# Kernel optimization log

Hardware: AMD Instinct MI355X
Metric: run time of the kernel (lower is better)

The kernel has to match this reference:

```python
import jax, jax.numpy as jnp
import numpy as np

N_NODES = 50000
N_EDGES = 400000
H = 128
L = 3
T = 2
FEAT = 4
N_DATA = 40000


def setup_inputs() -> dict:
    key = jax.random.key(0)
    ks = jax.random.split(key, 12)
    s = lambda k, shape, fan: jax.random.normal(k, shape, dtype=jnp.float32) / np.sqrt(fan)
    inp = {
        'x': jax.random.normal(ks[0], (N_NODES, FEAT), dtype=jnp.float32),
        'edge_index': jax.random.randint(ks[1], (2, N_EDGES), 0, N_NODES, dtype=jnp.int64) if jax.config.jax_enable_x64 else jax.random.randint(ks[1], (2, N_EDGES), 0, N_NODES).astype(jnp.int32),
        'edge_type': jax.random.randint(ks[2], (N_EDGES,), 0, T).astype(jnp.int32),
        'n_data': N_DATA,
        'W_in': s(ks[3], (FEAT, H), FEAT),
        'b_in': jnp.zeros((H,), jnp.float32),
        'W1': s(ks[4], (L, T, 2 * H, H), 2 * H),
        'b1': jnp.zeros((L, T, H), jnp.float32),
        'W2': s(ks[5], (L, T, H, H), H),
        'b2': jnp.zeros((L, T, H), jnp.float32),
        'W_ih': s(ks[6], (L, H, 3 * H), H),
        'b_ih': jnp.zeros((L, 3 * H), jnp.float32),
        'W_hh': s(ks[7], (L, H, 3 * H), H),
        'b_hh': jnp.zeros((L, 3 * H), jnp.float32),
        'Wr1': s(ks[8], (H, H), H),
        'br1': jnp.zeros((H,), jnp.float32),
        'Wr2': s(ks[9], (H, 1), H),
        'br2': jnp.zeros((1,), jnp.float32),
    }
    return inp


def _gru_cell(agg, h, W_ih, b_ih, W_hh, b_hh):
    # torch GRUCell: gates ordered (r, z, n)
    gi = agg @ W_ih + b_ih  # [N, 3H]
    gh = h @ W_hh + b_hh    # [N, 3H]
    i_r, i_z, i_n = jnp.split(gi, 3, axis=-1)
    h_r, h_z, h_n = jnp.split(gh, 3, axis=-1)
    r = jax.nn.sigmoid(i_r + h_r)
    z = jax.nn.sigmoid(i_z + h_z)
    n = jnp.tanh(i_n + r * h_n)
    return (1.0 - z) * n + z * h


def reference(x, edge_index, edge_type, n_data, W_in, b_in, W1, b1, W2, b2,
              W_ih, b_ih, W_hh, b_hh, Wr1, br1, Wr2, br2):
    num_nodes = x.shape[0]
    h = jax.nn.relu(x @ W_in + b_in)  # input_proj (dropout = identity in eval)
    src, dst = edge_index[0], edge_index[1]
    n_layers, n_types = W1.shape[0], W1.shape[1]
    for l in range(n_layers):
        cat = jnp.concatenate([h[src], h[dst]], axis=1)  # [E, 2H]
        msgs = jnp.zeros((cat.shape[0], h.shape[1]), dtype=h.dtype)
        for t in range(n_types):
            m_t = jax.nn.relu(cat @ W1[l, t] + b1[l, t]) @ W2[l, t] + b2[l, t]
            msgs = jnp.where((edge_type == t)[:, None], m_t, msgs)
        agg = jax.ops.segment_sum(msgs, dst, num_segments=num_nodes)  # scatter_add
        h = _gru_cell(agg, h, W_ih[l], b_ih[l], W_hh[l], b_hh[l])
    data_emb = h[:n_data]  # node_type==0 nodes are the first n_data nodes
    out = jax.nn.relu(data_emb @ Wr1 + br1) @ Wr2 + br2  # readout
    return out[:, 0]
```

## Files before the change

### kernel.cpp

```cpp
#include <hip/hip_runtime.h>
#include <math.h>


#define H 128
#define TE2 128
#define MS2 132
#define HS  136
#define FEAT 4
#define WG_PER_LAYER 196608
#define WR_TOTAL 32768

typedef __bf16 bf16x8 __attribute__((ext_vector_type(8)));
typedef __bf16 bf16x4 __attribute__((ext_vector_type(4)));
typedef float  f32x4  __attribute__((ext_vector_type(4)));

__global__ __launch_bounds__(256) void k_input(
    const float* __restrict__ x, const float* __restrict__ Win,
    const float* __restrict__ bin, float* __restrict__ h,
    __bf16* __restrict__ hb, int n_nodes)
{
    int idx = blockIdx.x * 256 + threadIdx.x;
    if (idx >= n_nodes * H) return;
    int n = idx >> 7, j = idx & 127;
    float acc = bin[j];
#pragma unroll
    for (int f = 0; f < FEAT; f++)
        acc += x[n * FEAT + f] * Win[f * H + j];
    float v = fmaxf(acc, 0.f);
    h[idx] = v;
    hb[idx] = (__bf16)v;
}

__global__ __launch_bounds__(256) void k_wconv(
    const float* __restrict__ W1, const float* __restrict__ W2,
    __bf16* __restrict__ Wsw)
{
    int gid = blockIdx.x * 256 + threadIdx.x;
    const int per_lt = 12 * 4096;
    if (gid >= 6 * per_lt) return;
    int lt = gid / per_lt, rem = gid % per_lt;
    int chunk = rem >> 12;
    int within = rem & 4095;
    int ct = within >> 9;
    int lane = (within >> 3) & 63;
    int j = within & 7;
    int r = lane & 15, quad = lane >> 4;
    int n = ct * 16 + r;
    float v;
    if (chunk < 8) {
        int k = chunk * 32 + quad * 8 + j;
        v = W1[((size_t)lt * 256 + k) * 128 + n];
    } else {
        int k = (chunk - 8) * 32 + quad * 8 + j;
        v = W2[((size_t)lt * 128 + k) * 128 + n];
    }
    Wsw[gid] = (__bf16)v;
}

__global__ __launch_bounds__(256) void k_wgconv(
    const float* __restrict__ Wih, const float* __restrict__ Whh,
    __bf16* __restrict__ Wg)
{
    int gid = blockIdx.x * 256 + threadIdx.x;
    if (gid >= 3 * WG_PER_LAYER) return;
    int layer = gid / WG_PER_LAYER, rem = gid % WG_PER_LAYER;
    int t = rem & 7;
    int lane = (rem >> 3) & 63;
    int jtg = (rem >> 9) % 24;
    int mk = rem / 12288;
    int kc = mk & 3;
    int msplit = mk >> 2;
    int mat = msplit >> 1, split = msplit & 1;
    int r = lane & 15, quad = lane >> 4;
    int k = kc * 32 + quad * 8 + t;
    int n = jtg * 16 + r;
    const float* W = (mat ? Whh : Wih) + (size_t)layer * 128 * 384;
    float v = W[(size_t)k * 384 + n];
    __bf16 hi = (__bf16)v;
    Wg[gid] = split ? (__bf16)(v - (float)hi) : hi;
}

__global__ __launch_bounds__(256) void k_wrconv(
    const float* __restrict__ Wr1, __bf16* __restrict__ Wr1s)
{
    int gid = blockIdx.x * 256 + threadIdx.x;
    if (gid >= WR_TOTAL) return;
    int t = gid & 7;
    int lane = (gid >> 3) & 63;
    int jtg = (gid >> 9) & 7;
    int kc = (gid >> 12) & 3;
    int split = gid >> 14;
    int r = lane & 15, quad = lane >> 4;
    int k = kc * 32 + quad * 8 + t;
    int n = jtg * 16 + r;
    float v = Wr1[(size_t)k * H + n];
    __bf16 hi = (__bf16)v;
    Wr1s[gid] = split ? (__bf16)(v - (float)hi) : hi;
}

__global__ __launch_bounds__(256) void k_hist(
    const int* __restrict__ et, const int* __restrict__ dst,
    int* __restrict__ cnt, int n_edges, int nn)
{
    int i = blockIdx.x * 256 + threadIdx.x;
    if (i < n_edges) atomicAdd(&cnt[et[i] * nn + dst[i]], 1);
}

__global__ __launch_bounds__(1024) void k_scan1(
    const int* __restrict__ cnt, int* __restrict__ bsum, int n)
{
    int i = blockIdx.x * 1024 + threadIdx.x;
    int v = (i < n) ? cnt[i] : 0;
#pragma unroll
    for (int off = 32; off > 0; off >>= 1) v += __shfl_down(v, off, 64);
    __shared__ int ws[16];
    int lane = threadIdx.x & 63, w = threadIdx.x >> 6;
    if (lane == 0) ws[w] = v;
    __syncthreads();
    if (threadIdx.x < 16) {
        int x = ws[threadIdx.x];
#pragma unroll
        for (int off = 8; off > 0; off >>= 1) x += __shfl_down(x, off, 64);
        if (threadIdx.x == 0) bsum[blockIdx.x] = x;
    }
}

__global__ __launch_bounds__(128) void k_scan2(
    int* __restrict__ bsum, int* __restrict__ offs, int nb, int n)
{
    int lane = threadIdx.x & 63, w = threadIdx.x >> 6;
    int v = (threadIdx.x < nb) ? bsum[threadIdx.x] : 0;
    int orig = v;
#pragma unroll
    for (int off = 1; off < 64; off <<= 1) {
        int t = __shfl_up(v, off, 64);
        if (lane >= off) v += t;
    }
    __shared__ int w0sum;
    if (threadIdx.x == 63) w0sum = v;
    __syncthreads();
    int ex = v - orig + (w ? w0sum : 0);
    if (threadIdx.x < nb) bsum[threadIdx.x] = ex;
    if (threadIdx.x == nb - 1) offs[n] = ex + orig;
}

__global__ __launch_bounds__(1024) void k_scan3(
    const int* __restrict__ cnt, const int* __restrict__ bsum,
    int* __restrict__ offs, int n)
{
    int i = blockIdx.x * 1024 + threadIdx.x;
    int v = (i < n) ? cnt[i] : 0;
    int orig = v;
    int lane = threadIdx.x & 63, w = threadIdx.x >> 6;
#pragma unroll
    for (int off = 1; off < 64; off <<= 1) {
        int t = __shfl_up(v, off, 64);
        if (lane >= off) v += t;
    }
    __shared__ int ws[16];
    if (lane == 63) ws[w] = v;
    __syncthreads();
    if (threadIdx.x < 16) {
        int x = ws[threadIdx.x];
#pragma unroll
        for (int off = 1; off < 16; off <<= 1) {
            int t = __shfl_up(x, off, 64);
            if (lane >= off) x += t;
        }
        ws[threadIdx.x] = x;
    }
    __syncthreads();
    int wbase = w ? ws[w - 1] : 0;
    if (i < n) offs[i] = bsum[blockIdx.x] + wbase + v - orig;
}

__global__ __launch_bounds__(256) void k_place(
    const int* __restrict__ et, const int* __restrict__ dst,
    const int* __restrict__ offs, int* __restrict__ cnt,
    int* __restrict__ bucket, int n_edges, int nn)
{
    int i = blockIdx.x * 256 + threadIdx.x;
    if (i < n_edges) {
        int key = et[i] * nn + dst[i];
        int p = atomicAdd(&cnt[key], -1) - 1;
        bucket[offs[key] + p] = i;
    }
}

__global__ __launch_bounds__(512, 4) void k_msg(
    const __bf16* __restrict__ hb,
    const int* __restrict__ bucket, const int* __restrict__ offs,
    const int* __restrict__ src, const int* __restrict__ dst,
    const __bf16* __restrict__ Wsw, const float* __restrict__ b1l,
    const float* __restrict__ b2l,
    float* __restrict__ agg, int n_edges, int nn)
{
    const int t = blockIdx.y;
    const int c0 = offs[nn];
    const int cnt = t ? (n_edges - c0) : c0;
    const int base = t ? c0 : 0;
    const int start = blockIdx.x * TE2;
    if (start >= cnt) return;

    const __bf16* __restrict__ W = Wsw + (size_t)t * 12 * 4096;
    const float*  __restrict__ b1 = b1l + t * H;
    const float*  __restrict__ b2 = b2l + t * H;

    __shared__ __bf16 sW[4096];
    __shared__ float  sMsg[TE2 * MS2];
    __shared__ int    sDstV[TE2];

    const int tid  = threadIdx.x;
    const int lane = tid & 63;
    const int w    = tid >> 6;
    const int r    = lane & 15;
    const int quad = lane >> 4;

    f32x4 wreg[12];
#pragma unroll
    for (int c = 0; c < 12; c++)
        wreg[c] = *(const f32x4*)(W + c * 4096 + tid * 8);

    if (tid < TE2) {
        int i = start + tid;
        sDstV[tid] = (i < cnt) ? dst[bucket[base + i]] : -1;
    }

    int ei = start + w * 16 + r;
    int e = bucket[base + (ei < cnt ? ei : cnt - 1)];
    const __bf16* aps = hb + (size_t)src[e] * H;
    const __bf16* apd = hb + (size_t)dst[e] * H;

    bf16x8 afS[4];
#pragma unroll
    for (int i = 0; i < 4; i++)
        afS[i] = *(const bf16x8*)(aps + i * 32 + quad * 8);

    __syncthreads();

    f32x4 acc[8];
#pragma unroll
    for (int ct = 0; ct < 8; ct++) acc[ct] = (f32x4){0.f, 0.f, 0.f, 0.f};

    bf16x8 afD[4];
#pragma unroll
    for (int kc = 0; kc < 8; kc++) {
        __syncthreads();
        *(f32x4*)(sW + tid * 8) = wreg[kc];
        __syncthreads();
        if (kc == 2) {
#pragma unroll
            for (int i = 0; i < 4; i++)
                afD[i] = *(const bf16x8*)(apd + i * 32 + quad * 8);
        }
        bf16x8 b = (kc < 4) ? afS[kc] : afD[kc - 4];
#pragma unroll
        for (int ct = 0; ct < 8; ct++) {
            bf16x8 a = *(const bf16x8*)(sW + ct * 512 + lane * 8);
            acc[ct] = __builtin_amdgcn_mfma_f32_16x16x32_bf16(a, b, acc[ct], 0, 0, 0);
        }
    }

    __bf16* sHid = (__bf16*)(sMsg + w * 16 * MS2);
#pragma unroll
    for (int ct = 0; ct < 8; ct++) {
        f32x4 bb4 = *(const f32x4*)(b1 + ct * 16 + quad * 4);
        bf16x4 hv;
#pragma unroll
        for (int g = 0; g < 4; g++)
            hv[g] = (__bf16)fmaxf(acc[ct][g] + bb4[g], 0.f);
        *(bf16x4*)(sHid + r * HS + ct * 16 + quad * 4) = hv;
    }

    f32x4 acc2[8];
#pragma unroll
    for (int ct = 0; ct < 8; ct++) acc2[ct] = (f32x4){0.f, 0.f, 0.f, 0.f};
#pragma unroll
    for (int kc = 0; kc < 4; kc++) {
        __syncthreads();
        *(f32x4*)(sW + tid * 8) = wreg[8 + kc];
        __syncthreads();
        bf16x8 b = *(const bf16x8*)(sHid + r * HS + kc * 32 + quad * 8);
#pragma unroll
        for (int ct = 0; ct < 8; ct++) {
            bf16x8 a = *(const bf16x8*)(sW + ct * 512 + lane * 8);
            acc2[ct] = __builtin_amdgcn_mfma_f32_16x16x32_bf16(a, b, acc2[ct], 0, 0, 0);
        }
    }

#pragma unroll
    for (int ct = 0; ct < 8; ct++) {
        f32x4 bb4 = *(const f32x4*)(b2 + ct * 16 + quad * 4);
        f32x4 mv;
#pragma unroll
        for (int g = 0; g < 4; g++)
            mv[g] = acc2[ct][g] + bb4[g];
        *(f32x4*)(sMsg + (w * 16 + r) * MS2 + ct * 16 + quad * 4) = mv;
    }
    __syncthreads();

    {
        int j = tid & 127, strip = tid >> 7;
        int e0 = strip * 32;
        float run = 0.f; int curd = -1;
        for (int q = 0; q < 32; q++) {
            int d = sDstV[e0 + q];
            float v = sMsg[(e0 + q) * MS2 + j];
            if (d != curd) {
                if (curd >= 0) atomicAdd(agg + (size_t)curd * H + j, run);
                run = 0.f; curd = d;
            }
            if (d >= 0) run += v;
        }
        if (curd >= 0) atomicAdd(agg + (size_t)curd * H + j, run);
    }
}

__global__ __launch_bounds__(512, 2) void k_gru(
    float* __restrict__ h, __bf16* __restrict__ hb,
    float* __restrict__ agg,
    const __bf16* __restrict__ Wg,
    const float* __restrict__ bih, const float* __restrict__ bhh,
    int n_nodes)
{
    const int nb = blockIdx.x * 32;
    const int tid = threadIdx.x;
    __shared__ __bf16 sIn[4][32][HS];

#pragma unroll
    for (int v = 0; v < 2; v++) {
        int idx = tid + 512 * v;
        int e = idx >> 5, c4 = (idx & 31) * 4;
        int n = nb + e;
        float4 av = {0.f, 0.f, 0.f, 0.f}, hv = {0.f, 0.f, 0.f, 0.f};
        if (n < n_nodes) {
            av = *(const float4*)(agg + (size_t)n * H + c4);
            hv = *(const float4*)(h + (size_t)n * H + c4);
            float4 z = {0.f, 0.f, 0.f, 0.f};
            *(float4*)(agg + (size_t)n * H + c4) = z;
        }
        bf16x4 ahi, alo, hhi, hlo;
        float af[4] = {av.x, av.y, av.z, av.w};
        float hf[4] = {hv.x, hv.y, hv.z, hv.w};
#pragma unroll
        for (int c = 0; c < 4; c++) {
            __bf16 ah = (__bf16)af[c]; ahi[c] = ah; alo[c] = (__bf16)(af[c] - (float)ah);
            __bf16 hh = (__bf16)hf[c]; hhi[c] = hh; hlo[c] = (__bf16)(hf[c] - (float)hh);
        }
        *(bf16x4*)&sIn[0][e][c4] = ahi;
        *(bf16x4*)&sIn[1][e][c4] = alo;
        *(bf16x4*)&sIn[2][e][c4] = hhi;
        *(bf16x4*)&sIn[3][e][c4] = hlo;
    }
    __syncthreads();

    const int lane = tid & 63, w = tid >> 6;
    const int r = lane & 15, quad = lane >> 4;
    const int jt = w;

    f32x4 acc[2][3][2];
#pragma unroll
    for (int m = 0; m < 2; m++)
#pragma unroll
        for (int g = 0; g < 3; g++)
#pragma unroll
            for (int mat = 0; mat < 2; mat++)
                acc[m][g][mat] = (f32x4){0.f, 0.f, 0.f, 0.f};

    bf16x8 B[2][12];
#pragma unroll
    for (int mat = 0; mat < 2; mat++)
#pragma unroll
    for (int g = 0; g < 3; g++)
#pragma unroll
    for (int sp = 0; sp < 2; sp++)
        B[0][mat * 6 + g * 2 + sp] = *(const bf16x8*)(Wg +
            ((((size_t)(mat * 2 + sp) * 4 + 0) * 24 + (g * 8 + jt)) * 64 + lane) * 8);

#pragma unroll
    for (int kc = 0; kc < 4; kc++) {
        const int cur = kc & 1, nxt = cur ^ 1;
        if (kc < 3) {
#pragma unroll
            for (int mat = 0; mat < 2; mat++)
#pragma unroll
            for (int g = 0; g < 3; g++)
#pragma unroll
            for (int sp = 0; sp < 2; sp++)
                B[nxt][mat * 6 + g * 2 + sp] = *(const bf16x8*)(Wg +
                    ((((size_t)(mat * 2 + sp) * 4 + (kc + 1)) * 24 + (g * 8 + jt)) * 64 + lane) * 8);
        }
        bf16x8 A[2][4];
#pragma unroll
        for (int m = 0; m < 2; m++)
#pragma unroll
            for (int s = 0; s < 4; s++)
                A[m][s] = *(const bf16x8*)&sIn[s][m * 16 + r][kc * 32 + quad * 8];
#pragma unroll
        for (int g = 0; g < 3; g++)
#pragma unroll
        for (int mat = 0; mat < 2; mat++) {
            bf16x8 bhi = B[cur][mat * 6 + g * 2 + 0];
            bf16x8 blo = B[cur][mat * 6 + g * 2 + 1];
            int s = mat * 2;
#pragma unroll
            for (int m = 0; m < 2; m++) {
                acc[m][g][mat] = __builtin_amdgcn_mfma_f32_16x16x32_bf16(
                    A[m][s], bhi, acc[m][g][mat], 0, 0, 0);
                acc[m][g][mat] = __builtin_amdgcn_mfma_f32_16x16x32_bf16(
                    A[m][s], blo, acc[m][g][mat], 0, 0, 0);
                acc[m][g][mat] = __builtin_amdgcn_mfma_f32_16x16x32_bf16(
                    A[m][s + 1], bhi, acc[m][g][mat], 0, 0, 0);
            }
        }
    }

    const int jcol = jt * 16 + r;
    float br_ = bih[jcol], bz_ = bih[128 + jcol], bn_ = bih[256 + jcol];
    float cr = bhh[jcol], cz = bhh[128 + jcol], cn = bhh[256 + jcol];
#pragma unroll
    for (int m = 0; m < 2; m++)
#pragma unroll
    for (int g4 = 0; g4 < 4; g4++) {
        int n = nb + m * 16 + quad * 4 + g4;
        if (n < n_nodes) {
            float ir = acc[m][0][0][g4], hr = acc[m][0][1][g4];
            float iz = acc[m][1][0][g4], hz = acc[m][1][1][g4];
            float in_ = acc[m][2][0][g4], hn = acc[m][2][1][g4];
            float hold = h[(size_t)n * H + jcol];
            float rr = 1.f / (1.f + expf(-(ir + br_ + hr + cr)));
            float zz = 1.f / (1.f + expf(-(iz + bz_ + hz + cz)));
            float nv = tanhf(in_ + bn_ + rr * (hn + cn));
            float out = (1.f - zz) * nv + zz * hold;
            h[(size_t)n * H + jcol] = out;
            hb[(size_t)n * H + jcol] = (__bf16)out;
        }
    }
}

__global__ __launch_bounds__(256, 4) void k_readout(
    const float* __restrict__ h, const __bf16* __restrict__ Wr1s,
    const float* __restrict__ br1, const float* __restrict__ Wr2,
    const float* __restrict__ br2, float* __restrict__ out, int n_out)
{
    const int nb = blockIdx.x * 32;
    const int tid = threadIdx.x;
    __shared__ __bf16 sIn[2][32][HS];
    __shared__ float sRed[4][32];

#pragma unroll
    for (int v = 0; v < 4; v++) {
        int idx = tid + 256 * v;
        int e = idx >> 5, c4 = (idx & 31) * 4;
        int n = nb + e;
        float4 hv = {0.f, 0.f, 0.f, 0.f};
        if (n < n_out)
            hv = *(const float4*)(h + (size_t)n * H + c4);
        float hf[4] = {hv.x, hv.y, hv.z, hv.w};
        bf16x4 hhi, hlo;
#pragma unroll
        for (int c = 0; c < 4; c++) {
            __bf16 hh = (__bf16)hf[c];
            hhi[c] = hh; hlo[c] = (__bf16)(hf[c] - (float)hh);
        }
        *(bf16x4*)&sIn[0][e][c4] = hhi;
        *(bf16x4*)&sIn[1][e][c4] = hlo;
    }
    __syncthreads();

    const int lane = tid & 63, w = tid >> 6;
    const int r = lane & 15, quad = lane >> 4;

    f32x4 acc[2][2];
#pragma unroll
    for (int m = 0; m < 2; m++)
#pragma unroll
        for (int j = 0; j < 2; j++)
            acc[m][j] = (f32x4){0.f, 0.f, 0.f, 0.f};

#pragma unroll
    for (int kc = 0; kc < 4; kc++) {
        bf16x8 A[2][2];
#pragma unroll
        for (int m = 0; m < 2; m++)
#pragma unroll
            for (int s = 0; s < 2; s++)
                A[m][s] = *(const bf16x8*)&sIn[s][m * 16 + r][kc * 32 + quad * 8];
#pragma unroll
        for (int j = 0; j < 2; j++) {
            int jtg = w * 2 + j;
            bf16x8 bhi = *(const bf16x8*)(Wr1s +
                ((size_t)(0 * 4 + kc) * 8 + jtg) * 512 + lane * 8);
            bf16x8 blo = *(const bf16x8*)(Wr1s +
                ((size_t)(1 * 4 + kc) * 8 + jtg) * 512 + lane * 8);
#pragma unroll
            for (int m = 0; m < 2; m++) {
                acc[m][j] = __builtin_amdgcn_mfma_f32_16x16x32_bf16(
                    A[m][0], bhi, acc[m][j], 0, 0, 0);
                acc[m][j] = __builtin_amdgcn_mfma_f32_16x16x32_bf16(
                    A[m][0], blo, acc[m][j], 0, 0, 0);
                acc[m][j] = __builtin_amdgcn_mfma_f32_16x16x32_bf16(
                    A[m][1], bhi, acc[m][j], 0, 0, 0);
            }
        }
    }

    float part[2][4];
#pragma unroll
    for (int m = 0; m < 2; m++)
#pragma unroll
        for (int g = 0; g < 4; g++) part[m][g] = 0.f;
#pragma unroll
    for (int j = 0; j < 2; j++) {
        int col = (w * 2 + j) * 16 + r;
        float b1v = br1[col], w2v = Wr2[col];
#pragma unroll
        for (int m = 0; m < 2; m++)
#pragma unroll
            for (int g = 0; g < 4; g++)
                part[m][g] += fmaxf(acc[m][j][g] + b1v, 0.f) * w2v;
    }
#pragma unroll
    for (int mask = 1; mask < 16; mask <<= 1)
#pragma unroll
        for (int m = 0; m < 2; m++)
#pragma unroll
            for (int g = 0; g < 4; g++)
                part[m][g] += __shfl_xor(part[m][g], mask, 16);
    if (r == 0) {
#pragma unroll
        for (int m = 0; m < 2; m++)
#pragma unroll
            for (int g = 0; g < 4; g++)
                sRed[w][m * 16 + quad * 4 + g] = part[m][g];
    }
    __syncthreads();
    if (tid < 32) {
        int n = nb + tid;
        if (n < n_out)
            out[n] = sRed[0][tid] + sRed[1][tid] + sRed[2][tid] + sRed[3][tid]
                     + br2[0];
    }
}

extern "C" void kernel_launch(void* const* d_in, const int* in_sizes, int n_in,
                              void* d_out, int out_size, void* d_ws, size_t ws_size,
                              hipStream_t stream)
{
    const float* x      = (const float*)d_in[0];
    const int*   eidx   = (const int*)d_in[1];
    const int*   etype  = (const int*)d_in[2];
    const float* Win    = (const float*)d_in[4];
    const float* bin    = (const float*)d_in[5];
    const float* W1     = (const float*)d_in[6];
    const float* b1     = (const float*)d_in[7];
    const float* W2     = (const float*)d_in[8];
    const float* b2     = (const float*)d_in[9];
    const float* Wih    = (const float*)d_in[10];
    const float* bih    = (const float*)d_in[11];
    const float* Whh    = (const float*)d_in[12];
    const float* bhh    = (const float*)d_in[13];
    const float* Wr1    = (const float*)d_in[14];
    const float* br1    = (const float*)d_in[15];
    const float* Wr2    = (const float*)d_in[16];
    const float* br2    = (const float*)d_in[17];

    const int n_nodes = in_sizes[0] / FEAT;
    const int n_edges = in_sizes[1] / 2;
    const int L = 3;
    const size_t nh = (size_t)n_nodes * H;

    const int* src = eidx;
    const int* dst = eidx + n_edges;

    float*  h    = (float*)d_ws;
    float*  agg  = h + nh;
    __bf16* hb   = (__bf16*)(agg + nh);
    __bf16* Wsw  = hb + nh;
    __bf16* Wg   = Wsw + 6 * 12 * 4096;
    __bf16* Wr1s = Wg + 3 * WG_PER_LAYER;
    int* bucket  = (int*)(Wr1s + WR_TOTAL);
    int* cnt     = bucket + n_edges;
    int* offs    = cnt + 2 * n_nodes;
    int* bsum    = offs + 2 * n_nodes + 1;

    const int nscan = 2 * n_nodes;
    const int nb = (nscan + 1023) / 1024;

    hipMemsetAsync(cnt, 0, (size_t)nscan * sizeof(int), stream);

    k_wconv<<<(6 * 12 * 4096 + 255) / 256, 256, 0, stream>>>(W1, W2, Wsw);
    k_wgconv<<<(3 * WG_PER_LAYER + 255) / 256, 256, 0, stream>>>(Wih, Whh, Wg);
    k_wrconv<<<(WR_TOTAL + 255) / 256, 256, 0, stream>>>(Wr1, Wr1s);
    k_input<<<((int)nh + 255) / 256, 256, 0, stream>>>(x, Win, bin, h, hb, n_nodes);

    const int eb = (n_edges + 255) / 256;
    k_hist <<<eb, 256, 0, stream>>>(etype, dst, cnt, n_edges, n_nodes);
    k_scan1<<<nb, 1024, 0, stream>>>(cnt, bsum, nscan);
    k_scan2<<<1, 128, 0, stream>>>(bsum, offs, nb, nscan);
    k_scan3<<<nb, 1024, 0, stream>>>(cnt, bsum, offs, nscan);
    k_place<<<eb, 256, 0, stream>>>(etype, dst, offs, cnt, bucket, n_edges, n_nodes);

    hipMemsetAsync(agg, 0, nh * sizeof(float), stream);

    const dim3 mgrid((n_edges + TE2 - 1) / TE2, 2);
    for (int l = 0; l < L; l++) {
        k_msg<<<mgrid, 512, 0, stream>>>(
            hb, bucket, offs, src, dst,
            Wsw + (size_t)l * 2 * 12 * 4096,
            b1 + (size_t)l * 2 * H, b2 + (size_t)l * 2 * H,
            agg, n_edges, n_nodes);
        k_gru<<<(n_nodes + 31) / 32, 512, 0, stream>>>(
            h, hb, agg,
            Wg + (size_t)l * WG_PER_LAYER,
            bih + (size_t)l * 384, bhh + (size_t)l * 384,
            n_nodes);
    }

    k_readout<<<(out_size + 31) / 32, 256, 0, stream>>>(
        h, Wr1s, br1, Wr2, br2, (float*)d_out, out_size);
}
```

Baseline: 573.6 us.

## Split GRU input and hidden matmuls across separate wavefronts with LDS exchange

The GRU kernel now launches 1024 threads per block, so each of 16 waves computes either the input-gate (agg·W_ih) or the hidden-gate (h·W_hh) product for one 16-column tile. Hidden-gate results are exchanged through shared memory, which reuses the input staging buffer, and the input-side waves apply the gate nonlinearities. This halves per-thread accumulators and B registers to raise occupancy and MFMA parallelism. The cost is an extra LDS round trip, two more block barriers, and half the waves sitting idle during the epilogue.

```diff
diff --git a/kernel.cpp b/kernel.cpp
--- a/kernel.cpp
+++ b/kernel.cpp
@@ -6,6 +6,7 @@
 #define TE2 128
 #define MS2 132
 #define HS  136
+#define EXS 132
 #define FEAT 4
 #define WG_PER_LAYER 196608
 #define WR_TOTAL 32768
@@ -316,7 +317,7 @@
     }
 }
 
-__global__ __launch_bounds__(512, 2) void k_gru(
+__global__ __launch_bounds__(1024, 4) void k_gru(
     float* __restrict__ h, __bf16* __restrict__ hb,
     float* __restrict__ agg,
     const __bf16* __restrict__ Wg,
@@ -325,12 +326,13 @@
 {
     const int nb = blockIdx.x * 32;
     const int tid = threadIdx.x;
-    __shared__ __bf16 sIn[4][32][HS];
-
-#pragma unroll
-    for (int v = 0; v < 2; v++) {
-        int idx = tid + 512 * v;
-        int e = idx >> 5, c4 = (idx & 31) * 4;
+
+    __shared__ char sRaw[3 * 32 * EXS * 4];
+    __bf16 (*sIn)[32][HS] = (__bf16(*)[32][HS])sRaw;
+    float* sEx = (float*)sRaw;
+
+    {
+        int e = tid >> 5, c4 = (tid & 31) * 4;
         int n = nb + e;
         float4 av = {0.f, 0.f, 0.f, 0.f}, hv = {0.f, 0.f, 0.f, 0.f};
         if (n < n_nodes) {
@@ -356,25 +358,22 @@
 
     const int lane = tid & 63, w = tid >> 6;
     const int r = lane & 15, quad = lane >> 4;
-    const int jt = w;
-
-    f32x4 acc[2][3][2];
+    const int jt = w & 7;
+    const int mat = w >> 3;
+
+    f32x4 acc[2][3];
 #pragma unroll
     for (int m = 0; m < 2; m++)
 #pragma unroll
         for (int g = 0; g < 3; g++)
-#pragma unroll
-            for (int mat = 0; mat < 2; mat++)
-                acc[m][g][mat] = (f32x4){0.f, 0.f, 0.f, 0.f};
-
-    bf16x8 B[2][12];
-#pragma unroll
-    for (int mat = 0; mat < 2; mat++)
+            acc[m][g] = (f32x4){0.f, 0.f, 0.f, 0.f};
+
+    bf16x8 B[2][6];
 #pragma unroll
     for (int g = 0; g < 3; g++)
 #pragma unroll
     for (int sp = 0; sp < 2; sp++)
-        B[0][mat * 6 + g * 2 + sp] = *(const bf16x8*)(Wg +
+        B[0][g * 2 + sp] = *(const bf16x8*)(Wg +
             ((((size_t)(mat * 2 + sp) * 4 + 0) * 24 + (g * 8 + jt)) * 64 + lane) * 8);
 
 #pragma unroll
@@ -382,58 +381,72 @@
         const int cur = kc & 1, nxt = cur ^ 1;
         if (kc < 3) {
 #pragma unroll
-            for (int mat = 0; mat < 2; mat++)
-#pragma unroll
             for (int g = 0; g < 3; g++)
 #pragma unroll
             for (int sp = 0; sp < 2; sp++)
-                B[nxt][mat * 6 + g * 2 + sp] = *(const bf16x8*)(Wg +
+                B[nxt][g * 2 + sp] = *(const bf16x8*)(Wg +
                     ((((size_t)(mat * 2 + sp) * 4 + (kc + 1)) * 24 + (g * 8 + jt)) * 64 + lane) * 8);
         }
-        bf16x8 A[2][4];
+        bf16x8 A[2][2];
 #pragma unroll
         for (int m = 0; m < 2; m++)
 #pragma unroll
-            for (int s = 0; s < 4; s++)
-                A[m][s] = *(const bf16x8*)&sIn[s][m * 16 + r][kc * 32 + quad * 8];
+            for (int s = 0; s < 2; s++)
+                A[m][s] = *(const bf16x8*)&sIn[mat * 2 + s][m * 16 + r][kc * 32 + quad * 8];
+#pragma unroll
+        for (int g = 0; g < 3; g++) {
+            bf16x8 bhi = B[cur][g * 2 + 0];
+            bf16x8 blo = B[cur][g * 2 + 1];
+#pragma unroll
+            for (int m = 0; m < 2; m++) {
+                acc[m][g] = __builtin_amdgcn_mfma_f32_16x16x32_bf16(
+                    A[m][0], bhi, acc[m][g], 0, 0, 0);
+                acc[m][g] = __builtin_amdgcn_mfma_f32_16x16x32_bf16(
+                    A[m][0], blo, acc[m][g], 0, 0, 0);
+                acc[m][g] = __builtin_amdgcn_mfma_f32_16x16x32_bf16(
+                    A[m][1], bhi, acc[m][g], 0, 0, 0);
+            }
+        }
+    }
+
+    __syncthreads();
+
+    const int jcol = jt * 16 + r;
+    if (mat == 1) {
+#pragma unroll
+        for (int m = 0; m < 2; m++)
 #pragma unroll
         for (int g = 0; g < 3; g++)
 #pragma unroll
-        for (int mat = 0; mat < 2; mat++) {
-            bf16x8 bhi = B[cur][mat * 6 + g * 2 + 0];
-            bf16x8 blo = B[cur][mat * 6 + g * 2 + 1];
-            int s = mat * 2;
-#pragma unroll
-            for (int m = 0; m < 2; m++) {
-                acc[m][g][mat] = __builtin_amdgcn_mfma_f32_16x16x32_bf16(
-                    A[m][s], bhi, acc[m][g][mat], 0, 0, 0);
-                acc[m][g][mat] = __builtin_amdgcn_mfma_f32_16x16x32_bf16(
-                    A[m][s], blo, acc[m][g][mat], 0, 0, 0);
-                acc[m][g][mat] = __builtin_amdgcn_mfma_f32_16x16x32_bf16(
-                    A[m][s + 1], bhi, acc[m][g][mat], 0, 0, 0);
+        for (int g4 = 0; g4 < 4; g4++) {
+            int e = m * 16 + quad * 4 + g4;
+            sEx[(g * 32 + e) * EXS + jcol] = acc[m][g][g4];
+        }
+    }
+    __syncthreads();
+
+    if (mat == 0) {
+        float br_ = bih[jcol], bz_ = bih[128 + jcol], bn_ = bih[256 + jcol];
+        float cr = bhh[jcol], cz = bhh[128 + jcol], cn = bhh[256 + jcol];
+#pragma unroll
+        for (int m = 0; m < 2; m++)
+#pragma unroll
+        for (int g4 = 0; g4 < 4; g4++) {
+            int e = m * 16 + quad * 4 + g4;
+            int n = nb + e;
+            if (n < n_nodes) {
+                float ir = acc[m][0][g4], iz = acc[m][1][g4], in_ = acc[m][2][g4];
+                float hr = sEx[(0 * 32 + e) * EXS + jcol];
+                float hz = sEx[(1 * 32 + e) * EXS + jcol];
+                float hn = sEx[(2 * 32 + e) * EXS + jcol];
+                float hold = h[(size_t)n * H + jcol];
+                float rr = 1.f / (1.f + expf(-(ir + br_ + hr + cr)));
+                float zz = 1.f / (1.f + expf(-(iz + bz_ + hz + cz)));
+                float nv = tanhf(in_ + bn_ + rr * (hn + cn));
+                float out = (1.f - zz) * nv + zz * hold;
+                h[(size_t)n * H + jcol] = out;
+                hb[(size_t)n * H + jcol] = (__bf16)out;
             }
-        }
-    }
-
-    const int jcol = jt * 16 + r;
-    float br_ = bih[jcol], bz_ = bih[128 + jcol], bn_ = bih[256 + jcol];
-    float cr = bhh[jcol], cz = bhh[128 + jcol], cn = bhh[256 + jcol];
-#pragma unroll
-    for (int m = 0; m < 2; m++)
-#pragma unroll
-    for (int g4 = 0; g4 < 4; g4++) {
-        int n = nb + m * 16 + quad * 4 + g4;
-        if (n < n_nodes) {
-            float ir = acc[m][0][0][g4], hr = acc[m][0][1][g4];
-            float iz = acc[m][1][0][g4], hz = acc[m][1][1][g4];
-            float in_ = acc[m][2][0][g4], hn = acc[m][2][1][g4];
-            float hold = h[(size_t)n * H + jcol];
-            float rr = 1.f / (1.f + expf(-(ir + br_ + hr + cr)));
-            float zz = 1.f / (1.f + expf(-(iz + bz_ + hz + cz)));
-            float nv = tanhf(in_ + bn_ + rr * (hn + cn));
-            float out = (1.f - zz) * nv + zz * hold;
-            h[(size_t)n * H + jcol] = out;
-            hb[(size_t)n * H + jcol] = (__bf16)out;
         }
     }
 }
@@ -610,7 +623,7 @@
             Wsw + (size_t)l * 2 * 12 * 4096,
             b1 + (size_t)l * 2 * H, b2 + (size_t)l * 2 * H,
             agg, n_edges, n_nodes);
-        k_gru<<<(n_nodes + 31) / 32, 512, 0, stream>>>(
+        k_gru<<<(n_nodes + 31) / 32, 1024, 0, stream>>>(
             h, hb, agg,
             Wg + (size_t)l * WG_PER_LAYER,
             bih + (size_t)l * 384, bhh + (size_t)l * 384,
```

After: 569.0 us. Within noise of the previous version (-0.8%).
